# Kernel tuning notes

Hardware: AMD Instinct MI355X
Metric: run time of the kernel (lower is better)

The kernel has to match this reference:

```python
import jax, jax.numpy as jnp
import numpy as np

B, C, T = 8, 1024, 1024
H, K, R = 8, 8, 8
DQK = C // K      # 128, per-head q/k channels
DFC1 = C // R     # 128, FC hidden
DINNER = C // H   # 128, per-head FC output


def setup_inputs() -> dict:
    key = jax.random.key(0)
    ks = jax.random.split(key, 12)
    s_in = 1.0 / np.sqrt(C)
    s_fc = 1.0 / np.sqrt(DFC1)
    return {
        "x": jax.random.normal(ks[0], (B, C, T), dtype=jnp.float32),
        # per-head 1x1 conv weights stacked over heads
        "Wq": jax.random.normal(ks[1], (H, DQK, C), dtype=jnp.float32) * s_in,
        "bq": jax.random.normal(ks[2], (H, DQK), dtype=jnp.float32) * 0.01,
        "Wk": jax.random.normal(ks[3], (H, DQK, C), dtype=jnp.float32) * s_in,
        "bk": jax.random.normal(ks[4], (H, DQK), dtype=jnp.float32) * 0.01,
        "Wv": jax.random.normal(ks[5], (H, C, C), dtype=jnp.float32) * s_in,
        "bv": jax.random.normal(ks[6], (H, C), dtype=jnp.float32) * 0.01,
        # gamma is zero-init in torch; use small random values to exercise the math
        "gamma": jax.random.normal(ks[7], (H,), dtype=jnp.float32) * 0.1,
        # post-concat MLP (nn.Linear weights, shape (out, in))
        "W1": jax.random.normal(ks[8], (DFC1, C), dtype=jnp.float32) * s_in,
        "b1": jax.random.normal(ks[9], (DFC1,), dtype=jnp.float32) * 0.01,
        "W2": jax.random.normal(ks[10], (DINNER, DFC1), dtype=jnp.float32) * s_fc,
        "b2": jax.random.normal(ks[11], (DINNER,), dtype=jnp.float32) * 0.01,
    }


def reference(x, Wq, bq, Wk, bk, Wv, bv, gamma, W1, b1, W2, b2):
    # x: (B, C, T). 1x1 Conv1d == channel-wise linear; batch all H heads at once.
    q = jnp.einsum('hoc,bct->bhot', Wq, x) + bq[None, :, :, None]  # (B,H,DQK,T)
    k = jnp.einsum('hoc,bct->bhot', Wk, x) + bk[None, :, :, None]  # (B,H,DQK,T)
    v = jnp.einsum('hoc,bct->bhot', Wv, x) + bv[None, :, :, None]  # (B,H,C,T)
    # energy[b,h,t,s] = q[:, :, :, t] . k[:, :, :, s]; softmax over s (no scaling, as in source)
    attn = jax.nn.softmax(jnp.einsum('bhot,bhos->bhts', q, k), axis=-1)  # (B,H,T,T)
    # out[b,h,c,t] = sum_s v[b,h,c,s] * attn[b,h,t,s]
    o = jnp.einsum('bhcs,bhts->bhct', v, attn)                     # (B,H,C,T)
    heads = gamma[None, :, None, None] * o + x[:, None, :, :]      # (B,H,C,T)
    # torch.stack(outs, 2): (B, C, H, T)
    out = heads.transpose(0, 2, 1, 3).reshape(B, C, H * T)
    out = out.transpose(0, 2, 1)                                   # (B, H*T, C)
    # fcs: Linear -> ReLU -> Dropout(eval: identity) -> Linear -> ReLU -> Dropout
    out = jax.nn.relu(out @ W1.T + b1)
    out = jax.nn.relu(out @ W2.T + b2)                             # (B, H*T, DINNER)
    out = out.transpose(0, 2, 1).reshape(B, DINNER * H, T)         # (B, C, T)
    return out + x
```

## Files before the change

### kernel.cpp

```cpp
#include <hip/hip_runtime.h>
#include <hip/hip_bf16.h>

typedef __hip_bfloat16 bf16;
typedef __attribute__((ext_vector_type(8))) __bf16 bf16x8;
typedef __attribute__((ext_vector_type(4))) float f32x4;

#define BM 128
#define BN 128

typedef const __attribute__((address_space(1))) void gvoid;
typedef __attribute__((address_space(3))) void lvoid;

template<int MODE, int TBK, int LAYOUT>
__global__ __launch_bounds__(256)
void gemm_nt(const bf16* __restrict__ A, long lda, long sAb, long sAh,
             const bf16* __restrict__ B, long ldb, long sBb, long sBh,
             void* __restrict__ Cv, long ldc, long sCb, long sCh,
             int K,
             const float* __restrict__ bias, long sBiasZ,
             const float* __restrict__ gamma,
             const bf16* __restrict__ xt, long ldxt,
             const float* __restrict__ xf)
{
    __shared__ bf16 As[BM * TBK];
    __shared__ bf16 Bs[BN * TBK];
    const int bxt = (LAYOUT == 2) ? (blockIdx.x >> 3) : blockIdx.x;
    const int zb  = (LAYOUT == 2) ? blockIdx.z : (blockIdx.z >> 3);
    const int zh  = (LAYOUT == 2) ? (blockIdx.x & 7) : (blockIdx.z & 7);
    const bf16* Ab = A + (long)zb * sAb + (long)zh * sAh + (long)blockIdx.y * BM * lda;
    const bf16* Bb = B + (long)zb * sBb + (long)zh * sBh + (long)bxt * BN * ldb;
    const int tid  = threadIdx.x;
    const int wave = tid >> 6, lane = tid & 63;
    const int col  = lane & 15, quad = lane >> 4;
    const int wm = (wave & 1) * 64, wn = (wave >> 1) * 64;
    constexpr int CPR = TBK / 8;
    constexpr int NSLOT = TBK / 16;
    constexpr int NX = TBK / 32;

    const bf16* aAddr[NSLOT];
    const bf16* bAddr[NSLOT];
    #pragma unroll
    for (int i = 0; i < NSLOT; ++i) {
        int cbase = i * 256 + wave * 64;
        int c = cbase + lane;
        int m = c / CPR;
        int j = c % CPR;
        int kch = ((j ^ (m & 7)) << 3);
        aAddr[i] = Ab + (long)m * lda + kch;
        bAddr[i] = Bb + (long)m * ldb + kch;
    }

    int offA[NX][4], offB[NX][4];
    #pragma unroll
    for (int x = 0; x < NX; ++x) {
        int kq = x * 4 + quad;
        #pragma unroll
        for (int mi = 0; mi < 4; ++mi) {
            int m = wm + mi * 16 + col;
            offA[x][mi] = m * TBK + ((kq ^ (m & 7)) << 3);
            int n = wn + mi * 16 + col;
            offB[x][mi] = n * TBK + ((kq ^ (n & 7)) << 3);
        }
    }

    f32x4 acc[4][4] = {};

    for (int k0 = 0; k0 < K; k0 += TBK) {
        __syncthreads();
        #pragma unroll
        for (int i = 0; i < NSLOT; ++i) {
            int cbase = i * 256 + wave * 64;
            __builtin_amdgcn_global_load_lds(
                (gvoid*)aAddr[i], (lvoid*)(As + cbase * 8), 16, 0, 0);
            __builtin_amdgcn_global_load_lds(
                (gvoid*)bAddr[i], (lvoid*)(Bs + cbase * 8), 16, 0, 0);
            aAddr[i] += TBK;
            bAddr[i] += TBK;
        }
        __syncthreads();
        #pragma unroll
        for (int x = 0; x < NX; ++x) {
            bf16x8 af[4], bfr[4];
            #pragma unroll
            for (int mi = 0; mi < 4; ++mi)
                af[mi] = *(const bf16x8*)(As + offA[x][mi]);
            #pragma unroll
            for (int ni = 0; ni < 4; ++ni)
                bfr[ni] = *(const bf16x8*)(Bs + offB[x][ni]);
            #pragma unroll
            for (int mi = 0; mi < 4; ++mi)
                #pragma unroll
                for (int ni = 0; ni < 4; ++ni)
                    acc[mi][ni] = __builtin_amdgcn_mfma_f32_16x16x32_bf16(
                        af[mi], bfr[ni], acc[mi][ni], 0, 0, 0);
        }
    }

    const long m0 = (long)blockIdx.y * BM + wm;
    const long n0 = (long)bxt * BN + wn;
    float g = 0.f;
    if (MODE == 3) g = gamma[zh];

    float bn[4];
    if constexpr (MODE == 1 || MODE == 4 || MODE == 5) {
        #pragma unroll
        for (int ni = 0; ni < 4; ++ni)
            bn[ni] = bias[n0 + ni * 16 + col];
    }

    #pragma unroll
    for (int mi = 0; mi < 4; ++mi) {
        #pragma unroll
        for (int ni = 0; ni < 4; ++ni) {
            long mb = m0 + mi * 16 + quad * 4;
            long n  = n0 + ni * 16 + col;
            if constexpr (MODE == 0) {
                bf16* cp = (bf16*)Cv + (long)zb * sCb + (long)zh * sCh + mb * ldc + n;
                const float* bp = bias + zh * sBiasZ + mb;
                #pragma unroll
                for (int r = 0; r < 4; ++r) {
                    float v = acc[mi][ni][r] + bp[r];
                    *cp = __float2bfloat16(v);
                    cp += ldc;
                }
            } else if constexpr (MODE == 1) {
                bf16* cp = (bf16*)Cv + mb * ldc + n;
                #pragma unroll
                for (int r = 0; r < 4; ++r) {
                    float v = acc[mi][ni][r] + bn[ni];
                    *cp = __float2bfloat16(v);
                    cp += ldc;
                }
            } else if constexpr (MODE == 3) {
                bf16* cp = (bf16*)Cv + (long)zb * sCb + (long)zh * sCh + mb * ldc + n;
                const bf16* xp = xt + (long)zb * 1048576 + mb * ldxt + n;
                #pragma unroll
                for (int r = 0; r < 4; ++r) {
                    float xv = __bfloat162float(*xp);
                    *cp = __float2bfloat16(g * acc[mi][ni][r] + xv);
                    cp += ldc;
                    xp += ldxt;
                }
            } else if constexpr (MODE == 4) {
                bf16* cp = (bf16*)Cv + mb * ldc + n;
                #pragma unroll
                for (int r = 0; r < 4; ++r) {
                    float v = acc[mi][ni][r] + bn[ni];
                    v = v > 0.f ? v : 0.f;
                    *cp = __float2bfloat16(v);
                    cp += ldc;
                }
            } else {
                #pragma unroll
                for (int r = 0; r < 4; ++r) {
                    long m = mb + r;
                    float v = acc[mi][ni][r] + bn[ni];
                    v = v > 0.f ? v : 0.f;
                    long bb = m >> 13, h = (m >> 10) & 7, t = m & 1023;
                    long oi = bb * 1048576 + (n * 8 + h) * 1024 + t;
                    ((float*)Cv)[oi] = v + xf[oi];
                }
            }
        }
    }
}

__global__ __launch_bounds__(256, 2)
void attn_fused(const bf16* __restrict__ qk, bf16* __restrict__ attn)
{
    constexpr int PAD = 1032;
    __shared__ __align__(16) char smraw[40960];
    __shared__ float red[2][4][32];
    bf16* Qs = (bf16*)smraw;
    bf16* Ks = (bf16*)(smraw + 8192);
    bf16* Sbuf = (bf16*)smraw;

    const int z = blockIdx.x;
    const int zb = z >> 3, zh = z & 7;
    const int t0 = blockIdx.y * 32;
    const int tid = threadIdx.x, w = tid >> 6, lane = tid & 63;
    const int col = lane & 15, quad = lane >> 4;

    const bf16* Qbase = qk + ((long)zb * 1024 + t0) * 2048 + zh * 256;
    const bf16* Kbase = qk + (long)zb * 1024 * 2048 + zh * 256 + 128;

    #pragma unroll
    for (int i = 0; i < 2; ++i) {
        int cbase = i * 256 + w * 64;
        int c = cbase + lane;
        int m = c >> 4, j = c & 15;
        __builtin_amdgcn_global_load_lds(
            (gvoid*)(Qbase + (long)m * 2048 + ((j ^ (m & 7)) << 3)),
            (lvoid*)(Qs + cbase * 8), 16, 0, 0);
    }
    __syncthreads();
    bf16x8 af[2][4];
    #pragma unroll
    for (int mi = 0; mi < 2; ++mi) {
        int m = mi * 16 + col;
        #pragma unroll
        for (int ki = 0; ki < 4; ++ki)
            af[mi][ki] = *(const bf16x8*)(Qs + m * 128 + ((((ki << 2) + quad) ^ (m & 7)) << 3));
    }

    f32x4 acc[2][16] = {};
    #pragma unroll
    for (int si = 0; si < 8; ++si) {
        __syncthreads();
        const bf16* Kb = Kbase + (long)si * 128 * 2048;
        #pragma unroll
        for (int i = 0; i < 8; ++i) {
            int cbase = i * 256 + w * 64;
            int c = cbase + lane;
            int m = c >> 4, j = c & 15;
            __builtin_amdgcn_global_load_lds(
                (gvoid*)(Kb + (long)m * 2048 + ((j ^ (m & 7)) << 3)),
                (lvoid*)(Ks + cbase * 8), 16, 0, 0);
        }
        __syncthreads();
        bf16x8 bfr[2][4];
        #pragma unroll
        for (int ni = 0; ni < 2; ++ni) {
            int n = w * 32 + ni * 16 + col;
            #pragma unroll
            for (int ki = 0; ki < 4; ++ki)
                bfr[ni][ki] = *(const bf16x8*)(Ks + n * 128 + ((((ki << 2) + quad) ^ (n & 7)) << 3));
        }
        #pragma unroll
        for (int ki = 0; ki < 4; ++ki)
            #pragma unroll
            for (int mi = 0; mi < 2; ++mi)
                #pragma unroll
                for (int ni = 0; ni < 2; ++ni)
                    acc[mi][si * 2 + ni] = __builtin_amdgcn_mfma_f32_16x16x32_bf16(
                        af[mi][ki], bfr[ni][ki], acc[mi][si * 2 + ni], 0, 0, 0);
    }

    float rmx[2][4], rinv[2][4];
    #pragma unroll
    for (int mi = 0; mi < 2; ++mi)
        #pragma unroll
        for (int r = 0; r < 4; ++r) {
            float mx = acc[mi][0][r];
            #pragma unroll
            for (int j = 1; j < 16; ++j) mx = fmaxf(mx, acc[mi][j][r]);
            #pragma unroll
            for (int off = 1; off < 16; off <<= 1) mx = fmaxf(mx, __shfl_xor(mx, off, 64));
            rmx[mi][r] = mx;
        }
    if (col == 0) {
        #pragma unroll
        for (int mi = 0; mi < 2; ++mi)
            #pragma unroll
            for (int r = 0; r < 4; ++r)
                red[0][w][mi * 16 + quad * 4 + r] = rmx[mi][r];
    }
    __syncthreads();
    #pragma unroll
    for (int mi = 0; mi < 2; ++mi)
        #pragma unroll
        for (int r = 0; r < 4; ++r) {
            int row = mi * 16 + quad * 4 + r;
            rmx[mi][r] = fmaxf(fmaxf(red[0][0][row], red[0][1][row]),
                               fmaxf(red[0][2][row], red[0][3][row]));
        }
    #pragma unroll
    for (int mi = 0; mi < 2; ++mi)
        #pragma unroll
        for (int r = 0; r < 4; ++r) {
            float s = 0.f;
            #pragma unroll
            for (int j = 0; j < 16; ++j) {
                acc[mi][j][r] = __expf(acc[mi][j][r] - rmx[mi][r]);
                s += acc[mi][j][r];
            }
            #pragma unroll
            for (int off = 1; off < 16; off <<= 1) s += __shfl_xor(s, off, 64);
            rinv[mi][r] = s;
        }
    if (col == 0) {
        #pragma unroll
        for (int mi = 0; mi < 2; ++mi)
            #pragma unroll
            for (int r = 0; r < 4; ++r)
                red[1][w][mi * 16 + quad * 4 + r] = rinv[mi][r];
    }
    __syncthreads();
    #pragma unroll
    for (int mi = 0; mi < 2; ++mi)
        #pragma unroll
        for (int r = 0; r < 4; ++r) {
            int row = mi * 16 + quad * 4 + r;
            float s4 = red[1][0][row] + red[1][1][row] + red[1][2][row] + red[1][3][row];
            rinv[mi][r] = 1.0f / s4;
        }

    bf16* dst = attn + ((long)(zb * 8 + zh)) * 1048576 + (long)t0 * 1024;
    #pragma unroll
    for (int mi = 0; mi < 2; ++mi) {
        __syncthreads();
        #pragma unroll
        for (int j = 0; j < 16; ++j) {
            int colb = (j >> 1) * 128 + w * 32 + (j & 1) * 16 + col;
            #pragma unroll
            for (int r = 0; r < 4; ++r) {
                int rowh = quad * 4 + r;
                Sbuf[rowh * PAD + colb] = __float2bfloat16(acc[mi][j][r] * rinv[mi][r]);
            }
        }
        __syncthreads();
        #pragma unroll
        for (int i = 0; i < 8; ++i) {
            int c = i * 256 + tid;
            int rowh = c >> 7, jj = c & 127;
            bf16x8 vv = *(const bf16x8*)(Sbuf + rowh * PAD + jj * 8);
            *(bf16x8*)(dst + (long)(mi * 16 + rowh) * 1024 + jj * 8) = vv;
        }
    }
}

__global__ __launch_bounds__(256)
void transpose_cast_x(const float* __restrict__ x, bf16* __restrict__ xt)
{
    __shared__ float tile[32][33];
    int b = blockIdx.z;
    int c0 = blockIdx.y * 32, t0 = blockIdx.x * 32;
    int tx = threadIdx.x & 31, ty = threadIdx.x >> 5;
    const float* xb = x + (long)b * 1024 * 1024;
    #pragma unroll
    for (int i = 0; i < 4; ++i) {
        int c = ty + i * 8;
        tile[c][tx] = xb[(long)(c0 + c) * 1024 + t0 + tx];
    }
    __syncthreads();
    bf16* xtb = xt + (long)b * 1024 * 1024;
    #pragma unroll
    for (int i = 0; i < 4; ++i) {
        int t = ty + i * 8;
        xtb[(long)(t0 + t) * 1024 + c0 + tx] = __float2bfloat16(tile[tx][t]);
    }
}

__global__ __launch_bounds__(256)
void cast_f2b(const float* __restrict__ in, bf16* __restrict__ out, long n)
{
    long i = (long)blockIdx.x * 256 + threadIdx.x;
    long stride = (long)gridDim.x * 256;
    for (; i < n; i += stride) out[i] = __float2bfloat16(in[i]);
}

__global__ __launch_bounds__(256)
void build_wqk(const float* __restrict__ Wq, const float* __restrict__ Wk,
               const float* __restrict__ bq, const float* __restrict__ bk,
               bf16* __restrict__ Wqk, float* __restrict__ biasqk)
{
    long i = (long)blockIdx.x * 256 + threadIdx.x;
    long r = i >> 10, c = i & 1023;
    long h = r >> 8, rr = r & 255;
    float v = (rr < 128) ? Wq[(h * 128 + rr) * 1024 + c]
                         : Wk[(h * 128 + (rr - 128)) * 1024 + c];
    Wqk[i] = __float2bfloat16(v);
    if (c == 0)
        biasqk[r] = (rr < 128) ? bq[h * 128 + rr] : bk[h * 128 + rr - 128];
}

extern "C" void kernel_launch(void* const* d_in, const int* in_sizes, int n_in,
                              void* d_out, int out_size, void* d_ws, size_t ws_size,
                              hipStream_t stream)
{
    const float* x     = (const float*)d_in[0];
    const float* Wq    = (const float*)d_in[1];
    const float* bq    = (const float*)d_in[2];
    const float* Wk    = (const float*)d_in[3];
    const float* bk    = (const float*)d_in[4];
    const float* Wv    = (const float*)d_in[5];
    const float* bv    = (const float*)d_in[6];
    const float* gamma = (const float*)d_in[7];
    const float* W1    = (const float*)d_in[8];
    const float* b1    = (const float*)d_in[9];
    const float* W2    = (const float*)d_in[10];
    const float* b2    = (const float*)d_in[11];
    float* out = (float*)d_out;

    char* base = (char*)d_ws;
    const long MB = 1048576;
    bf16*  xt   = (bf16*)(base);
    bf16*  Wvb  = (bf16*)(base + 16 * MB);
    bf16*  vbuf = (bf16*)(base + 32 * MB);
    bf16*  Wqk  = (bf16*)(base + 32 * MB);
    float* bqk  = (float*)(base + 36 * MB);
    bf16*  attb = (bf16*)(base + 96 * MB);
    bf16*  W1b  = (bf16*)(base + 96 * MB);
    bf16*  W2b  = (bf16*)(base + 96 * MB + 524288);
    bf16*  y1c  = (bf16*)(base + 97 * MB);
    bf16*  ot   = (bf16*)(base + 160 * MB);
    bf16*  qkt  = (bf16*)(base + 224 * MB);

    dim3 blk(256);
    transpose_cast_x<<<dim3(32, 32, 8), blk, 0, stream>>>(x, xt);
    build_wqk<<<8192, blk, 0, stream>>>(Wq, Wk, bq, bk, Wqk, bqk);
    cast_f2b<<<4096, blk, 0, stream>>>(Wv, Wvb, 8192ll * 1024);

    const long M1 = 1048576, M2 = 2097152, M8 = 8388608;

    gemm_nt<1, 64, 0><<<dim3(16, 64, 1), blk, 0, stream>>>(
        xt, 1024, 0, 0, Wqk, 1024, 0, 0, qkt, 2048, 0, 0, 1024,
        bqk, 0, nullptr, nullptr, 0, nullptr);

    for (int q = 0; q < 2; ++q) {
        const long b0 = (long)q * 4;
        const bf16* xtq = xt + b0 * M1;
        gemm_nt<0, 64, 2><<<dim3(64, 8, 4), blk, 0, stream>>>(
            Wvb, 1024, 0, M1, xtq, 1024, M1, 0, vbuf, 1024, M8, M1, 1024,
            bv, 1024, nullptr, nullptr, 0, nullptr);
        attn_fused<<<dim3(32, 32, 1), blk, 0, stream>>>(
            qkt + b0 * M2, attb);
        gemm_nt<3, 64, 2><<<dim3(64, 8, 4), blk, 0, stream>>>(
            attb, 1024, M8, M1, vbuf, 1024, M8, M1,
            ot, 1024, M8, M1, 1024,
            nullptr, 0, gamma, xtq, 1024, nullptr);
        cast_f2b<<<512, blk, 0, stream>>>(W1, W1b, 128 * 1024);
        cast_f2b<<<64, blk, 0, stream>>>(W2, W2b, 128 * 128);
        gemm_nt<4, 64, 0><<<dim3(1, 256, 1), blk, 0, stream>>>(
            ot, 1024, 0, 0, W1b, 1024, 0, 0, y1c, 128, 0, 0, 1024,
            b1, 0, nullptr, nullptr, 0, nullptr);
        gemm_nt<5, 128, 0><<<dim3(1, 256, 1), blk, 0, stream>>>(
            y1c, 128, 0, 0, W2b, 128, 0, 0, out + b0 * M1, 0, 0, 0, 128,
            b2, 0, nullptr, nullptr, 0, x + b0 * M1);
    }
}
```

Measured before the change: 702.4 us.

## Use 256x128 tile GEMM with triple-buffered LDS ring for V and PV

Adds a new 512-thread GEMM kernel with 256x128 output tiles, async global-to-LDS loads into a three-stage ring buffer, and XOR-swizzled LDS layout. It replaces the 128x128 gemm_nt for the V projection and the attention-times-V GEMMs, which dominate the FLOPs. Larger tiles raise arithmetic intensity and the ring overlaps loads with MFMA work. The cost is more LDS (about 144KB) and registers per block, so occupancy drops and the grid has half as many blocks.

```diff
diff --git a/kernel.cpp b/kernel.cpp
--- a/kernel.cpp
+++ b/kernel.cpp
@@ -10,6 +10,148 @@
 
 typedef const __attribute__((address_space(1))) void gvoid;
 typedef __attribute__((address_space(3))) void lvoid;
+
+template<int MODE>
+__global__ __launch_bounds__(512)
+void gemm256(const bf16* __restrict__ A, long lda, long sAb, long sAh,
+             const bf16* __restrict__ B, long ldb, long sBb, long sBh,
+             void* __restrict__ Cv, long ldc, long sCb, long sCh,
+             int K,
+             const float* __restrict__ bias, long sBiasZ,
+             const float* __restrict__ gamma,
+             const bf16* __restrict__ xt, long ldxt)
+{
+    __shared__ bf16 ring[3][(256 + 128) * 64];
+    const int nt4 = blockIdx.x >> 3;
+    const int zh  = blockIdx.x & 7;
+    const int zb  = blockIdx.z;
+    const bf16* Ab = A + (long)zb * sAb + (long)zh * sAh + (long)blockIdx.y * 256 * lda;
+    const bf16* Bb = B + (long)zb * sBb + (long)zh * sBh + (long)nt4 * 128 * ldb;
+    const int tid = threadIdx.x;
+    const int wave = tid >> 6, lane = tid & 63;
+    const int col = lane & 15, quad = lane >> 4;
+    const int wm = (wave >> 1) * 64, wn = (wave & 1) * 64;
+
+    const bf16* aAddr[4];
+    const bf16* bAddr[2];
+    int aDst[4], bDst[2];
+    #pragma unroll
+    for (int i = 0; i < 4; ++i) {
+        int cbase = i * 512 + wave * 64;
+        int c = cbase + lane;
+        int m = c >> 3, j = c & 7;
+        aAddr[i] = Ab + (long)m * lda + ((j ^ (m & 7)) << 3);
+        aDst[i] = cbase * 8;
+    }
+    #pragma unroll
+    for (int i = 0; i < 2; ++i) {
+        int cbase = i * 512 + wave * 64;
+        int c = cbase + lane;
+        int m = c >> 3, j = c & 7;
+        bAddr[i] = Bb + (long)m * ldb + ((j ^ (m & 7)) << 3);
+        bDst[i] = 16384 + cbase * 8;
+    }
+
+    int offA[2][4], offB[2][4];
+    #pragma unroll
+    for (int x = 0; x < 2; ++x) {
+        int kq = x * 4 + quad;
+        #pragma unroll
+        for (int mi = 0; mi < 4; ++mi) {
+            int m = wm + mi * 16 + col;
+            offA[x][mi] = m * 64 + ((kq ^ (m & 7)) << 3);
+            int n = wn + mi * 16 + col;
+            offB[x][mi] = 16384 + n * 64 + ((kq ^ (n & 7)) << 3);
+        }
+    }
+
+    f32x4 acc[4][4] = {};
+
+    auto STAGE = [&](int rb) {
+        bf16* base = &ring[rb][0];
+        #pragma unroll
+        for (int i = 0; i < 4; ++i) {
+            __builtin_amdgcn_global_load_lds((gvoid*)aAddr[i], (lvoid*)(base + aDst[i]), 16, 0, 0);
+            aAddr[i] += 64;
+        }
+        #pragma unroll
+        for (int i = 0; i < 2; ++i) {
+            __builtin_amdgcn_global_load_lds((gvoid*)bAddr[i], (lvoid*)(base + bDst[i]), 16, 0, 0);
+            bAddr[i] += 64;
+        }
+    };
+
+    const int NT = K >> 6;
+    STAGE(0);
+    STAGE(1);
+    asm volatile("s_waitcnt vmcnt(6)" ::: "memory");
+    __builtin_amdgcn_s_barrier();
+    __builtin_amdgcn_sched_barrier(0);
+
+    int rc = 0;
+    for (int t = 0; t < NT; ++t) {
+        int r2 = rc + 2; if (r2 >= 3) r2 -= 3;
+        if (t + 2 < NT) STAGE(r2);
+        const bf16* buf = &ring[rc][0];
+        #pragma unroll
+        for (int x = 0; x < 2; ++x) {
+            bf16x8 af[4], bfr[4];
+            #pragma unroll
+            for (int mi = 0; mi < 4; ++mi)
+                af[mi] = *(const bf16x8*)(buf + offA[x][mi]);
+            #pragma unroll
+            for (int ni = 0; ni < 4; ++ni)
+                bfr[ni] = *(const bf16x8*)(buf + offB[x][ni]);
+            #pragma unroll
+            for (int mi = 0; mi < 4; ++mi)
+                #pragma unroll
+                for (int ni = 0; ni < 4; ++ni)
+                    acc[mi][ni] = __builtin_amdgcn_mfma_f32_16x16x32_bf16(
+                        af[mi], bfr[ni], acc[mi][ni], 0, 0, 0);
+        }
+        if (t + 2 < NT)
+            asm volatile("s_waitcnt vmcnt(6)" ::: "memory");
+        else if (t + 1 < NT)
+            asm volatile("s_waitcnt vmcnt(0)" ::: "memory");
+        if (t + 1 < NT) {
+            __builtin_amdgcn_s_barrier();
+            __builtin_amdgcn_sched_barrier(0);
+        }
+        rc = rc + 1; if (rc >= 3) rc -= 3;
+    }
+
+    const long m0 = (long)blockIdx.y * 256 + wm;
+    const long n0 = (long)nt4 * 128 + wn;
+    float g = 0.f;
+    if (MODE == 3) g = gamma[zh];
+    #pragma unroll
+    for (int mi = 0; mi < 4; ++mi) {
+        #pragma unroll
+        for (int ni = 0; ni < 4; ++ni) {
+            long mb = m0 + mi * 16 + quad * 4;
+            long n  = n0 + ni * 16 + col;
+            if constexpr (MODE == 0) {
+                bf16* cp = (bf16*)Cv + (long)zb * sCb + (long)zh * sCh + mb * ldc + n;
+                const float* bp = bias + zh * sBiasZ + mb;
+                #pragma unroll
+                for (int r = 0; r < 4; ++r) {
+                    *cp = __float2bfloat16(acc[mi][ni][r] + bp[r]);
+                    cp += ldc;
+                }
+            } else {
+                bf16* cp = (bf16*)Cv + (long)zb * sCb + (long)zh * sCh + mb * ldc + n;
+                const bf16* xp = xt + (long)zb * 1048576 + mb * ldxt + n;
+                #pragma unroll
+                for (int r = 0; r < 4; ++r) {
+                    float xv = __bfloat162float(*xp);
+                    *cp = __float2bfloat16(g * acc[mi][ni][r] + xv);
+                    cp += ldc;
+                    xp += ldxt;
+                }
+            }
+        }
+    }
+}
 
 template<int MODE, int TBK, int LAYOUT>
 __global__ __launch_bounds__(256)
@@ -410,15 +552,15 @@
     for (int q = 0; q < 2; ++q) {
         const long b0 = (long)q * 4;
         const bf16* xtq = xt + b0 * M1;
-        gemm_nt<0, 64, 2><<<dim3(64, 8, 4), blk, 0, stream>>>(
+        gemm256<0><<<dim3(64, 4, 4), dim3(512), 0, stream>>>(
             Wvb, 1024, 0, M1, xtq, 1024, M1, 0, vbuf, 1024, M8, M1, 1024,
-            bv, 1024, nullptr, nullptr, 0, nullptr);
+            bv, 1024, nullptr, nullptr, 0);
         attn_fused<<<dim3(32, 32, 1), blk, 0, stream>>>(
             qkt + b0 * M2, attb);
-        gemm_nt<3, 64, 2><<<dim3(64, 8, 4), blk, 0, stream>>>(
+        gemm256<3><<<dim3(64, 4, 4), dim3(512), 0, stream>>>(
             attb, 1024, M8, M1, vbuf, 1024, M8, M1,
             ot, 1024, M8, M1, 1024,
-            nullptr, 0, gamma, xtq, 1024, nullptr);
+            nullptr, 0, gamma, xtq, 1024);
         cast_f2b<<<512, blk, 0, stream>>>(W1, W1b, 128 * 1024);
         cast_f2b<<<64, blk, 0, stream>>>(W2, W2b, 128 * 128);
         gemm_nt<4, 64, 0><<<dim3(1, 256, 1), blk, 0, stream>>>(
```

After: 676.7 us. 1.04x faster.

## Add 256x256 8-wave pipelined GEMM kernel for QK, V and attention-V products

Applied to the files above, without the earlier changes.

Adds a new GEMM kernel that uses 512 threads and 256x256 output tiles. Operands are loaded directly from global memory into XOR-swizzled LDS through global_load_lds, in a four-slot ping-pong schedule. MFMA quadrants are interleaved with barriers and setprio so that loads overlap with compute. The kernel replaces the 128x128 gemm_nt for the QK projection, the V projection and the attn*V GEMM, aiming for more data reuse and better MFMA utilisation. The price is higher register and LDS pressure and a hand-scheduled barrier pattern that is fragile.

```diff
diff --git a/kernel.cpp b/kernel.cpp
--- a/kernel.cpp
+++ b/kernel.cpp
@@ -10,6 +10,190 @@
 
 typedef const __attribute__((address_space(1))) void gvoid;
 typedef __attribute__((address_space(3))) void lvoid;
+
+#define G8_BAR()  __builtin_amdgcn_s_barrier()
+#define G8_LGKM() do { asm volatile("s_waitcnt lgkmcnt(0)" ::: "memory"); \
+                       __builtin_amdgcn_sched_barrier(0); } while (0)
+#define G8_LDA(SLOT) do { \
+    _Pragma("unroll") for (int mi_ = 0; mi_ < 4; ++mi_) \
+    _Pragma("unroll") for (int ks_ = 0; ks_ < 2; ++ks_) \
+        af[mi_][ks_] = *(const bf16x8*)(lds + (SLOT) * 8192 + offA[mi_][ks_]); } while (0)
+#define G8_LDB(SLOT, BF) do { \
+    _Pragma("unroll") for (int ni_ = 0; ni_ < 2; ++ni_) \
+    _Pragma("unroll") for (int ks_ = 0; ks_ < 2; ++ks_) \
+        BF[ni_][ks_] = *(const bf16x8*)(lds + 32768 + (SLOT) * 8192 + offB[ni_][ks_]); } while (0)
+#define G8_STA(SLOT, HF, T) do { \
+    __builtin_amdgcn_global_load_lds((gvoid*)(Ab + aoff0 + (HF) * halfA + (T) * 64), \
+        (lvoid*)(lds + (SLOT) * 8192 + wave * 512), 16, 0, 0); \
+    __builtin_amdgcn_global_load_lds((gvoid*)(Ab + aoff1 + (HF) * halfA + (T) * 64), \
+        (lvoid*)(lds + (SLOT) * 8192 + 4096 + wave * 512), 16, 0, 0); } while (0)
+#define G8_STB(SLOT, HF, T) do { \
+    __builtin_amdgcn_global_load_lds((gvoid*)(Bb + boff0 + (HF) * halfB + (T) * 64), \
+        (lvoid*)(lds + 32768 + (SLOT) * 8192 + wave * 512), 16, 0, 0); \
+    __builtin_amdgcn_global_load_lds((gvoid*)(Bb + boff1 + (HF) * halfB + (T) * 64), \
+        (lvoid*)(lds + 32768 + (SLOT) * 8192 + 4096 + wave * 512), 16, 0, 0); } while (0)
+#define G8_MM(QM, QN, BF) do { \
+    _Pragma("unroll") for (int ks_ = 0; ks_ < 2; ++ks_) \
+    _Pragma("unroll") for (int mi_ = 0; mi_ < 4; ++mi_) \
+    _Pragma("unroll") for (int ni_ = 0; ni_ < 2; ++ni_) \
+        acc[QM][mi_][QN][ni_] = __builtin_amdgcn_mfma_f32_16x16x32_bf16( \
+            af[mi_][ks_], BF[ni_][ks_], acc[QM][mi_][QN][ni_], 0, 0, 0); } while (0)
+#define G8_VM(MORE) do { if (MORE) asm volatile("s_waitcnt vmcnt(4)" ::: "memory"); \
+                         else      asm volatile("s_waitcnt vmcnt(0)" ::: "memory"); } while (0)
+
+template<int MODE, int QKLAY>
+__global__ __launch_bounds__(512, 2)
+void gemm8p(const bf16* __restrict__ A, long lda, long sAb, long sAh,
+            const bf16* __restrict__ B, long ldb, long sBb, long sBh,
+            void* __restrict__ Cv, long ldc, long sCb, long sCh,
+            int K,
+            const float* __restrict__ bias, long sBiasZ,
+            const float* __restrict__ gamma,
+            const bf16* __restrict__ xt, long ldxt)
+{
+    __shared__ bf16 lds[65536];
+    const int mt = QKLAY ? (blockIdx.x >> 3) : ((blockIdx.x >> 3) >> 2);
+    const int nt = QKLAY ? (blockIdx.x & 7) : ((blockIdx.x >> 3) & 3);
+    const int zh = QKLAY ? 0 : (blockIdx.x & 7);
+    const int zb = QKLAY ? 0 : blockIdx.z;
+    const bf16* Ab = A + (long)zb * sAb + (long)zh * sAh + (long)mt * 256 * lda;
+    const bf16* Bb = B + (long)zb * sBb + (long)zh * sBh + (long)nt * 256 * ldb;
+    const int tid = threadIdx.x;
+    const int wave = tid >> 6, lane = tid & 63;
+    const int col16 = lane & 15, quad = lane >> 4;
+    const int wave_m = wave >> 2, wave_n = wave & 3;
+    const long halfA = 128 * lda, halfB = 128 * ldb;
+
+    long aoff0, aoff1, boff0, boff1;
+    {
+        int c0 = tid, c1 = 512 + tid;
+        int r0 = c0 >> 3, r1 = c1 >> 3;
+        aoff0 = (long)r0 * lda + (((c0 & 7) ^ (r0 & 7)) << 3);
+        aoff1 = (long)r1 * lda + (((c1 & 7) ^ (r1 & 7)) << 3);
+        boff0 = (long)r0 * ldb + (((c0 & 7) ^ (r0 & 7)) << 3);
+        boff1 = (long)r1 * ldb + (((c1 & 7) ^ (r1 & 7)) << 3);
+    }
+
+    int offA[4][2], offB[2][2];
+    #pragma unroll
+    for (int mi = 0; mi < 4; ++mi) {
+        int r = wave_m * 64 + mi * 16 + col16;
+        #pragma unroll
+        for (int ks = 0; ks < 2; ++ks)
+            offA[mi][ks] = r * 64 + ((((ks << 2) + quad) ^ (r & 7)) << 3);
+    }
+    #pragma unroll
+    for (int ni = 0; ni < 2; ++ni) {
+        int r = wave_n * 32 + ni * 16 + col16;
+        #pragma unroll
+        for (int ks = 0; ks < 2; ++ks)
+            offB[ni][ks] = r * 64 + ((((ks << 2) + quad) ^ (r & 7)) << 3);
+    }
+
+    f32x4 acc[2][4][2][2] = {};
+    bf16x8 af[4][2], bf0[2][2], bf1[2][2];
+
+    G8_STA(0, 0, 0);
+    G8_STB(0, 0, 0);
+    G8_STB(1, 1, 0);
+    G8_STA(1, 1, 0);
+    G8_STA(2, 0, 1);
+    G8_STB(3, 1, 1);
+    asm volatile("s_waitcnt vmcnt(4)" ::: "memory");
+    G8_BAR();
+
+    const int NIT = K >> 7;
+    for (int I = 0; I < NIT; ++I) {
+        const int t1 = 2 * I + 1;
+        const bool more = (I + 1 < NIT);
+        G8_LDA(0); G8_LDB(0, bf0);
+        G8_STA(3, 1, t1);
+        G8_BAR(); G8_LGKM();
+        __builtin_amdgcn_s_setprio(1); G8_MM(0, 0, bf0); __builtin_amdgcn_s_setprio(0);
+        G8_BAR();
+        G8_LDB(1, bf1);
+        G8_STB(2, 0, t1);
+        G8_BAR(); G8_LGKM();
+        __builtin_amdgcn_s_setprio(1); G8_MM(0, 1, bf1); __builtin_amdgcn_s_setprio(0);
+        G8_BAR();
+        G8_LDA(1);
+        if (more) G8_STA(0, 0, t1 + 1);
+        G8_BAR(); G8_LGKM();
+        __builtin_amdgcn_s_setprio(1); G8_MM(1, 1, bf1); __builtin_amdgcn_s_setprio(0);
+        G8_BAR();
+        if (more) G8_STB(1, 1, t1 + 1);
+        G8_BAR();
+        __builtin_amdgcn_s_setprio(1); G8_MM(1, 0, bf0); __builtin_amdgcn_s_setprio(0);
+        G8_VM(more);
+        G8_BAR();
+        G8_LDA(2); G8_LDB(2, bf0);
+        if (more) G8_STA(1, 1, t1 + 1);
+        G8_BAR(); G8_LGKM();
+        __builtin_amdgcn_s_setprio(1); G8_MM(0, 0, bf0); __builtin_amdgcn_s_setprio(0);
+        G8_BAR();
+        G8_LDB(3, bf1);
+        if (more) G8_STB(0, 0, t1 + 1);
+        G8_BAR(); G8_LGKM();
+        __builtin_amdgcn_s_setprio(1); G8_MM(0, 1, bf1); __builtin_amdgcn_s_setprio(0);
+        G8_BAR();
+        G8_LDA(3);
+        if (more) G8_STA(2, 0, t1 + 2);
+        G8_BAR(); G8_LGKM();
+        __builtin_amdgcn_s_setprio(1); G8_MM(1, 1, bf1); __builtin_amdgcn_s_setprio(0);
+        G8_BAR();
+        if (more) G8_STB(3, 1, t1 + 2);
+        G8_BAR();
+        __builtin_amdgcn_s_setprio(1); G8_MM(1, 0, bf0); __builtin_amdgcn_s_setprio(0);
+        G8_VM(more);
+        G8_BAR();
+    }
+
+    const long m0 = (long)mt * 256 + wave_m * 64;
+    const long n0 = (long)nt * 256 + wave_n * 32;
+    float g = 0.f;
+    if (MODE == 3) g = gamma[zh];
+    #pragma unroll
+    for (int qm = 0; qm < 2; ++qm) {
+        #pragma unroll
+        for (int mi = 0; mi < 4; ++mi) {
+            #pragma unroll
+            for (int qn = 0; qn < 2; ++qn) {
+                #pragma unroll
+                for (int ni = 0; ni < 2; ++ni) {
+                    long mb = m0 + qm * 128 + mi * 16 + quad * 4;
+                    long n  = n0 + qn * 128 + ni * 16 + col16;
+                    if constexpr (MODE == 0) {
+                        bf16* cp = (bf16*)Cv + (long)zb * sCb + (long)zh * sCh + mb * ldc + n;
+                        const float* bp = bias + zh * sBiasZ + mb;
+                        #pragma unroll
+                        for (int r = 0; r < 4; ++r) {
+                            *cp = __float2bfloat16(acc[qm][mi][qn][ni][r] + bp[r]);
+                            cp += ldc;
+                        }
+                    } else if constexpr (MODE == 1) {
+                        float bn = bias[n];
+                        bf16* cp = (bf16*)Cv + mb * ldc + n;
+                        #pragma unroll
+                        for (int r = 0; r < 4; ++r) {
+                            *cp = __float2bfloat16(acc[qm][mi][qn][ni][r] + bn);
+                            cp += ldc;
+                        }
+                    } else {
+                        bf16* cp = (bf16*)Cv + (long)zb * sCb + (long)zh * sCh + mb * ldc + n;
+                        const bf16* xp = xt + (long)zb * 1048576 + mb * ldxt + n;
+                        #pragma unroll
+                        for (int r = 0; r < 4; ++r) {
+                            float xv = __bfloat162float(*xp);
+                            *cp = __float2bfloat16(g * acc[qm][mi][qn][ni][r] + xv);
+                            cp += ldc;
+                            xp += ldxt;
+                        }
+                    }
+                }
+            }
+        }
+    }
+}
 
 template<int MODE, int TBK, int LAYOUT>
 __global__ __launch_bounds__(256)
@@ -403,22 +587,22 @@
 
     const long M1 = 1048576, M2 = 2097152, M8 = 8388608;
 
-    gemm_nt<1, 64, 0><<<dim3(16, 64, 1), blk, 0, stream>>>(
+    gemm8p<1, 1><<<dim3(256, 1, 1), dim3(512), 0, stream>>>(
         xt, 1024, 0, 0, Wqk, 1024, 0, 0, qkt, 2048, 0, 0, 1024,
-        bqk, 0, nullptr, nullptr, 0, nullptr);
+        bqk, 0, nullptr, nullptr, 0);
 
     for (int q = 0; q < 2; ++q) {
         const long b0 = (long)q * 4;
         const bf16* xtq = xt + b0 * M1;
-        gemm_nt<0, 64, 2><<<dim3(64, 8, 4), blk, 0, stream>>>(
+        gemm8p<0, 0><<<dim3(128, 1, 4), dim3(512), 0, stream>>>(
             Wvb, 1024, 0, M1, xtq, 1024, M1, 0, vbuf, 1024, M8, M1, 1024,
-            bv, 1024, nullptr, nullptr, 0, nullptr);
+            bv, 1024, nullptr, nullptr, 0);
         attn_fused<<<dim3(32, 32, 1), blk, 0, stream>>>(
             qkt + b0 * M2, attb);
-        gemm_nt<3, 64, 2><<<dim3(64, 8, 4), blk, 0, stream>>>(
+        gemm8p<3, 0><<<dim3(128, 1, 4), dim3(512), 0, stream>>>(
             attb, 1024, M8, M1, vbuf, 1024, M8, M1,
             ot, 1024, M8, M1, 1024,
-            nullptr, 0, gamma, xtq, 1024, nullptr);
+            nullptr, 0, gamma, xtq, 1024);
         cast_f2b<<<512, blk, 0, stream>>>(W1, W1b, 128 * 1024);
         cast_f2b<<<64, blk, 0, stream>>>(W2, W2b, 128 * 128);
         gemm_nt<4, 64, 0><<<dim3(1, 256, 1), blk, 0, stream>>>(
```

New measurement: 623.5 us. -11.2%, faster.
